# Performance work log

Hardware: AMD Instinct MI355X
Metric: run time of the kernel (lower is better)

Reference implementation:

```python
import jax, jax.numpy as jnp
import numpy as np

N_NODES = 100000
N_EDGES = 1600000
D_IN = 256
D_OUT = 128


def setup_inputs() -> dict:
    key = jax.random.key(0)
    k1, k2, k3, k4, k5, k6 = jax.random.split(key, 6)
    x = jax.random.normal(k1, (N_NODES, D_IN), dtype=jnp.float32)
    edge_src = jax.random.randint(k2, (N_EDGES,), 0, N_NODES, dtype=jnp.int32)
    edge_dst = jax.random.randint(k3, (N_EDGES,), 0, N_NODES, dtype=jnp.int32)
    edge_w = jax.random.uniform(k4, (N_EDGES,), dtype=jnp.float32)
    # GraphConvolution parameters (glorot-style scale)
    W = jax.random.normal(k5, (D_IN, D_OUT), dtype=jnp.float32) / np.sqrt(D_IN)
    b = jax.random.normal(k6, (D_OUT,), dtype=jnp.float32) * 0.01
    return {"x": x, "edge_src": edge_src, "edge_dst": edge_dst,
            "edge_w": edge_w, "W": W, "b": b}


def reference(x, edge_src, edge_dst, edge_w, W, b):
    # GraphConvolution: out = adj @ (x @ W) + b, adj given as weighted edge list
    support = x @ W                                   # [N, D_OUT] dense GEMM
    msgs = support[edge_src] * edge_w[:, None]        # [E, D_OUT] gather + scale
    out = jax.ops.segment_sum(msgs, edge_dst, num_segments=N_NODES)  # scatter-add
    return out + b
```

## Files before the change

### kernel.cpp

```cpp
#include <hip/hip_runtime.h>

#define N_NODES 100000
#define N_EDGES 1600000
#define D_IN 256
#define D_OUT 128

#define NPB 128
#define NB 782
#define REGION 2432
#define CHUNK 4096
#define NCHUNK 391
#define GEMM_BLOCKS 782

typedef __attribute__((ext_vector_type(8))) short bf16x8;
typedef __attribute__((ext_vector_type(4))) float f32x4;

__device__ __forceinline__ unsigned short f2bf(float f) {
    unsigned u = __float_as_uint(f);
    u += 0x7FFF + ((u >> 16) & 1);
    return (unsigned short)(u >> 16);
}
__device__ __forceinline__ float bflo(unsigned p) { return __uint_as_float(p << 16); }
__device__ __forceinline__ float bfhi(unsigned p) { return __uint_as_float(p & 0xFFFF0000u); }

__global__ void prep_kernel(const float* __restrict__ W,
                            unsigned short* __restrict__ Wt,
                            int* __restrict__ gcursor) {
    int idx = blockIdx.x * 256 + threadIdx.x;
    if (idx < D_OUT * D_IN) {
        int c = idx >> 8;
        int k = idx & 255;
        Wt[idx] = f2bf(W[(size_t)k * D_OUT + c]);
    }
    if (idx < NB) gcursor[idx] = 0;
}

struct BinSmem {
    int hist[NB];
    int startsh[NB];
    int adj[NB];
    int scanbuf[512];
    short sbin[CHUNK];
    int2 stage[CHUNK];
};
struct GemmSmem {
    unsigned short tile[8][16 * 136];
};
union FusedSmem { BinSmem b; GemmSmem g; };

__global__ __launch_bounds__(512) void fused_kernel(
        const float* __restrict__ x,
        const unsigned short* __restrict__ Wt,
        unsigned short* __restrict__ supb,
        const int* __restrict__ src,
        const int* __restrict__ dst,
        const float* __restrict__ ew,
        int* __restrict__ gcursor,
        int2* __restrict__ stg) {
    __shared__ FusedSmem sm;
    int tid = threadIdx.x;

    if (blockIdx.x < NCHUNK) {
        BinSmem& bs = sm.b;
        int e0 = blockIdx.x * CHUNK;
        int cn = N_EDGES - e0;
        if (cn > CHUNK) cn = CHUNK;

        for (int i = tid; i < NB; i += 512) bs.hist[i] = 0;
        __syncthreads();

        int2 tup[8];
        int bin[8];
#pragma unroll
        for (int k = 0; k < 8; ++k) {
            int e = e0 + k * 512 + tid;
            bin[k] = -1;
            if (e < N_EDGES) {
                int d = dst[e];
                bin[k] = d >> 7;
                tup[k] = make_int2(src[e] | ((d & 127) << 17),
                                   __float_as_int(ew[e]));
                atomicAdd(&bs.hist[bin[k]], 1);
            }
        }
        __syncthreads();

        int total0 = 0;
        for (int half = 0; half < 2; ++half) {
            int idx = half * 512 + tid;
            int v = (idx < NB) ? bs.hist[idx] : 0;
            bs.scanbuf[tid] = v;
            __syncthreads();
            for (int d = 1; d < 512; d <<= 1) {
                int t = (tid >= d) ? bs.scanbuf[tid - d] : 0;
                __syncthreads();
                bs.scanbuf[tid] += t;
                __syncthreads();
            }
            if (idx < NB) {
                int st = total0 + bs.scanbuf[tid] - v;
                bs.startsh[idx] = st;
                bs.adj[idx] = st;
            }
            total0 += bs.scanbuf[511];
            __syncthreads();
        }

#pragma unroll
        for (int k = 0; k < 8; ++k) {
            if (bin[k] >= 0) {
                int pos = atomicAdd(&bs.adj[bin[k]], 1);
                bs.stage[pos] = tup[k];
                bs.sbin[pos] = (short)bin[k];
            }
        }
        __syncthreads();

        for (int i = tid; i < NB; i += 512) {
            int hv = bs.hist[i];
            if (hv > 0)
                bs.adj[i] = atomicAdd(&gcursor[i], hv) - bs.startsh[i];
        }
        __syncthreads();

        for (int i = tid; i < cn; i += 512) {
            int bb = bs.sbin[i];
            int off = bs.adj[bb] + i;
            if (off < REGION)
                stg[(size_t)bb * REGION + off] = bs.stage[i];
        }
    } else {
        GemmSmem& gs = sm.g;
        int gb = blockIdx.x - NCHUNK;
        int widl = tid >> 6;
        int lane = tid & 63;
        int r0 = (gb * 8 + widl) * 16;
        int rowA = r0 + (lane & 15);
        int rowAc = rowA < N_NODES ? rowA : N_NODES - 1;
        int kgrp = (lane >> 4) * 8;

        f32x4 acc[8];
#pragma unroll
        for (int t = 0; t < 8; ++t) acc[t] = (f32x4){0.f, 0.f, 0.f, 0.f};

        const float* xrow = x + (size_t)rowAc * D_IN + kgrp;
        int colbase = lane & 15;

#pragma unroll
        for (int ks = 0; ks < 8; ++ks) {
            int k0 = ks * 32;
            float4 a0 = *(const float4*)(xrow + k0);
            float4 a1 = *(const float4*)(xrow + k0 + 4);
            bf16x8 afrag;
            afrag[0] = (short)f2bf(a0.x); afrag[1] = (short)f2bf(a0.y);
            afrag[2] = (short)f2bf(a0.z); afrag[3] = (short)f2bf(a0.w);
            afrag[4] = (short)f2bf(a1.x); afrag[5] = (short)f2bf(a1.y);
            afrag[6] = (short)f2bf(a1.z); afrag[7] = (short)f2bf(a1.w);
#pragma unroll
            for (int t = 0; t < 8; ++t) {
                bf16x8 bfrag = *(const bf16x8*)(Wt +
                        (size_t)(t * 16 + colbase) * D_IN + k0 + kgrp);
                acc[t] = __builtin_amdgcn_mfma_f32_16x16x32_bf16(afrag, bfrag,
                                                                 acc[t], 0, 0, 0);
            }
        }

        unsigned short* tl = gs.tile[widl];
        int rgrp = (lane >> 4) * 4;
#pragma unroll
        for (int t = 0; t < 8; ++t)
#pragma unroll
            for (int j = 0; j < 4; ++j)
                tl[(rgrp + j) * 136 + t * 16 + colbase] = f2bf(acc[t][j]);

        int row = lane >> 2;
        int c4 = lane & 3;
        int orow = r0 + row;
        if (orow < N_NODES) {
#pragma unroll
            for (int u = 0; u < 4; ++u) {
                int col0 = u * 32 + c4 * 8;
                int4 v = *(const int4*)(tl + row * 136 + col0);
                *(int4*)(supb + (size_t)orow * D_OUT + col0) = v;
            }
        }
    }
}

__global__ __launch_bounds__(512) void sgather_kernel(
        const unsigned short* __restrict__ supb,
        const int2* __restrict__ stg,
        const int* __restrict__ gcursor,
        const float* __restrict__ b,
        float* __restrict__ out) {
    __shared__ int2 sorted[REGION];
    __shared__ int hist2[NPB];
    __shared__ int base2[NPB + 1];
    __shared__ int cur2[NPB];
    __shared__ int scanbuf[512];

    int tid = threadIdx.x;
    int bkt = blockIdx.x;
    int node0 = bkt * NPB;

    if (tid < NPB) hist2[tid] = 0;
    __syncthreads();

    int cnt = gcursor[bkt];
    if (cnt > REGION) cnt = REGION;
    const int2* sg = stg + (size_t)bkt * REGION;

    int2 tp[5];
    int dl[5];
#pragma unroll
    for (int k = 0; k < 5; ++k) {
        int e = tid + k * 512;
        dl[k] = -1;
        if (e < cnt) {
            tp[k] = sg[e];
            dl[k] = (tp[k].x >> 17) & 127;
            atomicAdd(&hist2[dl[k]], 1);
        }
    }
    __syncthreads();

    int v = (tid < NPB) ? hist2[tid] : 0;
    scanbuf[tid] = v;
    __syncthreads();
    for (int d = 1; d < NPB; d <<= 1) {
        int t = (tid >= d) ? scanbuf[tid - d] : 0;
        __syncthreads();
        scanbuf[tid] += t;
        __syncthreads();
    }
    if (tid < NPB) {
        base2[tid] = scanbuf[tid] - v;
        cur2[tid] = scanbuf[tid] - v;
    }
    if (tid == 0) base2[NPB] = cnt;
    __syncthreads();

#pragma unroll
    for (int k = 0; k < 5; ++k) {
        if (dl[k] >= 0) {
            int pos = atomicAdd(&cur2[dl[k]], 1);
            sorted[pos] = tp[k];
        }
    }
    __syncthreads();

    int wave = tid >> 6, lane = tid & 63;
    float2 bv = ((const float2*)b)[lane];

#pragma unroll 1
    for (int jj = 0; jj < 16; ++jj) {
        int j = wave * 16 + jj;
        int node = node0 + j;
        if (node >= N_NODES) break;
        int s = base2[j], t = base2[j + 1];
        float ax = 0.f, ay = 0.f;
        int e = s;
        for (; e + 3 < t; e += 4) {
            int2 t0 = sorted[e];
            int2 t1 = sorted[e + 1];
            int2 t2 = sorted[e + 2];
            int2 t3 = sorted[e + 3];
            unsigned p0 = *(const unsigned*)(supb + (size_t)(t0.x & 0x1FFFF) * D_OUT + 2 * lane);
            unsigned p1 = *(const unsigned*)(supb + (size_t)(t1.x & 0x1FFFF) * D_OUT + 2 * lane);
            unsigned p2 = *(const unsigned*)(supb + (size_t)(t2.x & 0x1FFFF) * D_OUT + 2 * lane);
            unsigned p3 = *(const unsigned*)(supb + (size_t)(t3.x & 0x1FFFF) * D_OUT + 2 * lane);
            float w0 = __int_as_float(t0.y);
            float w1 = __int_as_float(t1.y);
            float w2 = __int_as_float(t2.y);
            float w3 = __int_as_float(t3.y);
            ax += w0 * bflo(p0) + w1 * bflo(p1) + w2 * bflo(p2) + w3 * bflo(p3);
            ay += w0 * bfhi(p0) + w1 * bfhi(p1) + w2 * bfhi(p2) + w3 * bfhi(p3);
        }
        for (; e < t; ++e) {
            int2 t0 = sorted[e];
            unsigned p0 = *(const unsigned*)(supb + (size_t)(t0.x & 0x1FFFF) * D_OUT + 2 * lane);
            float w0 = __int_as_float(t0.y);
            ax += w0 * bflo(p0);
            ay += w0 * bfhi(p0);
        }
        ((float2*)(out + (size_t)node * D_OUT))[lane] =
            make_float2(ax + bv.x, ay + bv.y);
    }
}

extern "C" void kernel_launch(void* const* d_in, const int* in_sizes, int n_in,
                              void* d_out, int out_size, void* d_ws, size_t ws_size,
                              hipStream_t stream) {
    const float* x   = (const float*)d_in[0];
    const int* esrc  = (const int*)d_in[1];
    const int* edst  = (const int*)d_in[2];
    const float* ew  = (const float*)d_in[3];
    const float* W   = (const float*)d_in[4];
    const float* b   = (const float*)d_in[5];
    float* out = (float*)d_out;

    uint8_t* w8 = (uint8_t*)d_ws;
    unsigned short* supb = (unsigned short*)w8;
    int2* stg     = (int2*)(w8 + 25600000);
    int*  gcursor = (int*)(w8 + 40814592);
    unsigned short* Wt = (unsigned short*)(w8 + 40818688);

    prep_kernel<<<(D_OUT * D_IN + 255) / 256, 256, 0, stream>>>(W, Wt, gcursor);

    fused_kernel<<<NCHUNK + GEMM_BLOCKS, 512, 0, stream>>>(
        x, Wt, supb, esrc, edst, ew, gcursor, stg);

    sgather_kernel<<<NB, 512, 0, stream>>>(supb, stg, gcursor, b, out);
}
```

Before: 301.8 us.

## Replace atomic-cursor binning with count/scan/flush three-pass bucketing

The single fused binning pass, which built a local sort, did a block-wide shared scan and claimed global slots with atomics, is split into three passes. A per-chunk histogram pass runs alongside the GEMM, a column scan over chunks computes deterministic start offsets, and a flush pass scatters edges directly to their slots using shared atomic cursors. This removes the heavy in-block scan, the staging buffers and the global atomics from the GEMM-overlapped kernel. In exchange it adds two kernel launches, reads the dst/src/ew arrays a second time, and the flush writes scattered rather than coalesced.

```diff
diff --git a/kernel.cpp b/kernel.cpp
--- a/kernel.cpp
+++ b/kernel.cpp
@@ -24,111 +24,41 @@
 __device__ __forceinline__ float bfhi(unsigned p) { return __uint_as_float(p & 0xFFFF0000u); }
 
 __global__ void prep_kernel(const float* __restrict__ W,
-                            unsigned short* __restrict__ Wt,
-                            int* __restrict__ gcursor) {
+                            unsigned short* __restrict__ Wt) {
     int idx = blockIdx.x * 256 + threadIdx.x;
     if (idx < D_OUT * D_IN) {
         int c = idx >> 8;
         int k = idx & 255;
         Wt[idx] = f2bf(W[(size_t)k * D_OUT + c]);
     }
-    if (idx < NB) gcursor[idx] = 0;
-}
-
-struct BinSmem {
-    int hist[NB];
-    int startsh[NB];
-    int adj[NB];
-    int scanbuf[512];
-    short sbin[CHUNK];
-    int2 stage[CHUNK];
-};
-struct GemmSmem {
-    unsigned short tile[8][16 * 136];
-};
-union FusedSmem { BinSmem b; GemmSmem g; };
-
-__global__ __launch_bounds__(512) void fused_kernel(
+}
+
+struct CountSmem { int hist[NB]; };
+struct GemmSmem { unsigned short tile[8][16 * 136]; };
+union FusedSmem { CountSmem c; GemmSmem g; };
+
+__global__ __launch_bounds__(512) void fusedA_kernel(
         const float* __restrict__ x,
         const unsigned short* __restrict__ Wt,
         unsigned short* __restrict__ supb,
-        const int* __restrict__ src,
         const int* __restrict__ dst,
-        const float* __restrict__ ew,
-        int* __restrict__ gcursor,
-        int2* __restrict__ stg) {
+        int* __restrict__ counts) {
     __shared__ FusedSmem sm;
     int tid = threadIdx.x;
 
     if (blockIdx.x < NCHUNK) {
-        BinSmem& bs = sm.b;
+        int* hist = sm.c.hist;
         int e0 = blockIdx.x * CHUNK;
-        int cn = N_EDGES - e0;
-        if (cn > CHUNK) cn = CHUNK;
-
-        for (int i = tid; i < NB; i += 512) bs.hist[i] = 0;
+        for (int i = tid; i < NB; i += 512) hist[i] = 0;
         __syncthreads();
-
-        int2 tup[8];
-        int bin[8];
 #pragma unroll
         for (int k = 0; k < 8; ++k) {
             int e = e0 + k * 512 + tid;
-            bin[k] = -1;
-            if (e < N_EDGES) {
-                int d = dst[e];
-                bin[k] = d >> 7;
-                tup[k] = make_int2(src[e] | ((d & 127) << 17),
-                                   __float_as_int(ew[e]));
-                atomicAdd(&bs.hist[bin[k]], 1);
-            }
+            if (e < N_EDGES) atomicAdd(&hist[dst[e] >> 7], 1);
         }
         __syncthreads();
-
-        int total0 = 0;
-        for (int half = 0; half < 2; ++half) {
-            int idx = half * 512 + tid;
-            int v = (idx < NB) ? bs.hist[idx] : 0;
-            bs.scanbuf[tid] = v;
-            __syncthreads();
-            for (int d = 1; d < 512; d <<= 1) {
-                int t = (tid >= d) ? bs.scanbuf[tid - d] : 0;
-                __syncthreads();
-                bs.scanbuf[tid] += t;
-                __syncthreads();
-            }
-            if (idx < NB) {
-                int st = total0 + bs.scanbuf[tid] - v;
-                bs.startsh[idx] = st;
-                bs.adj[idx] = st;
-            }
-            total0 += bs.scanbuf[511];
-            __syncthreads();
-        }
-
-#pragma unroll
-        for (int k = 0; k < 8; ++k) {
-            if (bin[k] >= 0) {
-                int pos = atomicAdd(&bs.adj[bin[k]], 1);
-                bs.stage[pos] = tup[k];
-                bs.sbin[pos] = (short)bin[k];
-            }
-        }
-        __syncthreads();
-
-        for (int i = tid; i < NB; i += 512) {
-            int hv = bs.hist[i];
-            if (hv > 0)
-                bs.adj[i] = atomicAdd(&gcursor[i], hv) - bs.startsh[i];
-        }
-        __syncthreads();
-
-        for (int i = tid; i < cn; i += 512) {
-            int bb = bs.sbin[i];
-            int off = bs.adj[bb] + i;
-            if (off < REGION)
-                stg[(size_t)bb * REGION + off] = bs.stage[i];
-        }
+        int* crow = counts + (size_t)blockIdx.x * NB;
+        for (int i = tid; i < NB; i += 512) crow[i] = hist[i];
     } else {
         GemmSmem& gs = sm.g;
         int gb = blockIdx.x - NCHUNK;
@@ -187,10 +117,62 @@
     }
 }
 
+__global__ __launch_bounds__(512) void scanB_kernel(
+        const int* __restrict__ counts,
+        int* __restrict__ starts,
+        int* __restrict__ totals) {
+    int wv = threadIdx.x >> 6, lane = threadIdx.x & 63;
+    int bin = blockIdx.x * 8 + wv;
+    if (bin >= NB) return;
+    int carry = 0;
+#pragma unroll
+    for (int g = 0; g < 7; ++g) {
+        int idx = g * 64 + lane;
+        int v = (idx < NCHUNK) ? counts[(size_t)idx * NB + bin] : 0;
+        int s = v;
+#pragma unroll
+        for (int d = 1; d < 64; d <<= 1) {
+            int u = __shfl_up(s, d, 64);
+            if (lane >= d) s += u;
+        }
+        if (idx < NCHUNK) starts[(size_t)idx * NB + bin] = carry + s - v;
+        carry += __shfl(s, 63, 64);
+    }
+    if (lane == 0) totals[bin] = carry;
+}
+
+__global__ __launch_bounds__(512) void flushC_kernel(
+        const int* __restrict__ src,
+        const int* __restrict__ dst,
+        const float* __restrict__ ew,
+        const int* __restrict__ starts,
+        int2* __restrict__ stg) {
+    __shared__ int cur[NB];
+    int tid = threadIdx.x;
+    int e0 = blockIdx.x * CHUNK;
+
+    const int* srow = starts + (size_t)blockIdx.x * NB;
+    for (int i = tid; i < NB; i += 512) cur[i] = srow[i];
+    __syncthreads();
+
+#pragma unroll
+    for (int k = 0; k < 8; ++k) {
+        int e = e0 + k * 512 + tid;
+        if (e < N_EDGES) {
+            int d = dst[e];
+            int bin = d >> 7;
+            int pos = atomicAdd(&cur[bin], 1);
+            if (pos < REGION)
+                stg[(size_t)bin * REGION + pos] =
+                    make_int2(src[e] | ((d & 127) << 17), __float_as_int(ew[e]));
+        }
+    }
+}
+
 __global__ __launch_bounds__(512) void sgather_kernel(
         const unsigned short* __restrict__ supb,
         const int2* __restrict__ stg,
-        const int* __restrict__ gcursor,
+        const int* __restrict__ totals,
         const float* __restrict__ b,
         float* __restrict__ out) {
     __shared__ int2 sorted[REGION];
@@ -206,7 +188,7 @@
     if (tid < NPB) hist2[tid] = 0;
     __syncthreads();
 
-    int cnt = gcursor[bkt];
+    int cnt = totals[bkt];
     if (cnt > REGION) cnt = REGION;
     const int2* sg = stg + (size_t)bkt * REGION;
 
@@ -301,14 +283,20 @@
 
     uint8_t* w8 = (uint8_t*)d_ws;
     unsigned short* supb = (unsigned short*)w8;
-    int2* stg     = (int2*)(w8 + 25600000);
-    int*  gcursor = (int*)(w8 + 40814592);
-    unsigned short* Wt = (unsigned short*)(w8 + 40818688);
-
-    prep_kernel<<<(D_OUT * D_IN + 255) / 256, 256, 0, stream>>>(W, Wt, gcursor);
-
-    fused_kernel<<<NCHUNK + GEMM_BLOCKS, 512, 0, stream>>>(
-        x, Wt, supb, esrc, edst, ew, gcursor, stg);
-
-    sgather_kernel<<<NB, 512, 0, stream>>>(supb, stg, gcursor, b, out);
-}
+    int2* stg    = (int2*)(w8 + 25600000);
+    int* counts  = (int*)(w8 + 40814592);
+    int* starts  = (int*)(w8 + 42037640);
+    int* totals  = (int*)(w8 + 43260688);
+    unsigned short* Wt = (unsigned short*)(w8 + 43264000);
+
+    prep_kernel<<<(D_OUT * D_IN + 255) / 256, 256, 0, stream>>>(W, Wt);
+
+    fusedA_kernel<<<NCHUNK + GEMM_BLOCKS, 512, 0, stream>>>(
+        x, Wt, supb, edst, counts);
+
+    scanB_kernel<<<(NB + 7) / 8, 512, 0, stream>>>(counts, starts, totals);
+
+    flushC_kernel<<<NCHUNK, 512, 0, stream>>>(esrc, edst, ew, starts, stg);
+
+    sgather_kernel<<<NB, 512, 0, stream>>>(supb, stg, totals, b, out);
+}
```

Result: slower. 329.4 us (+9.1%).
